# Optimization experiments

Measured on AMD Instinct MI355X. Metric: run time of the kernel, lower is better.

The kernel has to match this reference:

```python
import jax, jax.numpy as jnp
import numpy as np

B, L, K, H = 4, 256, 256, 768
KEY_SIZE, VAL_SIZE = 50000, 10000


def setup_inputs() -> dict:
    key = jax.random.key(0)
    k1, k2, k3, k4, k5, k6 = jax.random.split(key, 6)
    return {
        "hidden_state": jax.random.normal(k1, (B, L, H), dtype=jnp.float32),
        "key_seq": jax.random.randint(k2, (B, K), 0, KEY_SIZE),
        "value_matrix": jax.random.randint(k3, (B, L, K), 0, VAL_SIZE),
        "key_mask_matrix": jax.random.randint(k4, (B, L, K), 0, 2),
        "key_emb_table": jax.random.normal(k5, (KEY_SIZE, H), dtype=jnp.float32),
        "val_emb_table": jax.random.normal(k6, (VAL_SIZE, H), dtype=jnp.float32),
    }


def reference(hidden_state, key_seq, value_matrix, key_mask_matrix,
              key_emb_table, val_emb_table):
    temper = jnp.asarray(H, jnp.float32) ** 0.5
    # embedding lookups
    embedding_key = key_emb_table[key_seq]            # [B, K, H]
    embedding_val = val_emb_table[value_matrix]       # [B, L, K, H]
    # scores: hidden [B,L,H] x key [B,K,H] -> [B,L,K]
    u = jnp.einsum('blh,bkh->blk', hidden_state, embedding_key) / temper
    mask = jnp.clip(key_mask_matrix, 0, 1).astype(jnp.float32)
    delta_exp_u = jnp.exp(u) * mask                   # masked exp
    sum_delta = jnp.sum(delta_exp_u, axis=2, keepdims=True)
    p = delta_exp_u / (sum_delta + 1e-10)             # masked softmax [B,L,K]
    # weighted value sum (avoids the original's [H,B,L,K] broadcast+permute)
    o = jnp.einsum('blk,blkh->blh', p, embedding_val)
    return o + hidden_state
```

## Files before the change

kernel.cpp:

```cpp
#include <hip/hip_runtime.h>
#include <math.h>

typedef float    f32x2 __attribute__((ext_vector_type(2)));
typedef float    f32x4 __attribute__((ext_vector_type(4)));
typedef _Float16 f16x2 __attribute__((ext_vector_type(2)));

static constexpr int B_ = 4;
static constexpr int L_ = 256;
static constexpr int K_ = 256;
static constexpr int H_ = 768;
static constexpr int H2_ = H_ / 2;
static constexpr int VAL_SIZE_ = 10000;
static constexpr float INV_TEMPER = 0.03608439182435161f;

__device__ __forceinline__ unsigned pack_f16x2(float a, float b) {
  f16x2 p = {(_Float16)a, (_Float16)b};
  return __builtin_bit_cast(unsigned, p);
}
__device__ __forceinline__ float fdot2u(unsigned a, unsigned b, float c) {
#if __has_builtin(__builtin_amdgcn_fdot2)
  return __builtin_amdgcn_fdot2(__builtin_bit_cast(f16x2, a),
                                __builtin_bit_cast(f16x2, b), c, false);
#else
  f16x2 va = __builtin_bit_cast(f16x2, a);
  f16x2 vb = __builtin_bit_cast(f16x2, b);
  return c + (float)va.x * (float)vb.x + (float)va.y * (float)vb.y;
#endif
}

__device__ __forceinline__ float4 nt_load4(const float* p) {
  f32x4 v = __builtin_nontemporal_load(reinterpret_cast<const f32x4*>(p));
  return make_float4(v.x, v.y, v.z, v.w);
}

#if __has_builtin(__builtin_amdgcn_cvt_pk_fp8_f32)
#define HW_FP8_ENC 1
#endif
#if __has_builtin(__builtin_amdgcn_cvt_pk_f32_fp8)
#define HW_FP8_DEC 1
#endif

__device__ __forceinline__ unsigned fp8_enc1(float f) {
  unsigned s = (__float_as_uint(f) >> 31) << 7;
  float af = fminf(fabsf(f), 448.0f);
  unsigned em;
  if (af < 0.015625f) {
    em = (unsigned)rintf(af * 512.0f);
  } else {
    unsigned m = __float_as_uint(af);
    m += 0x7ffffu + ((m >> 20) & 1u);
    em = (m >> 20) - (120u << 3);
  }
  return s | em;
}
__device__ __forceinline__ float fp8_dec1(unsigned b) {
  unsigned em = b & 0x7fu;
  unsigned sbit = (b & 0x80u) << 24;
  float n = __uint_as_float(sbit | ((em + 960u) << 20));
  float sub = __uint_as_float(sbit | 0x3F800000u) * (float)em * 0.001953125f;
  return em >= 8u ? n : sub;
}
__device__ __forceinline__ unsigned fp8_enc4(float a, float b, float c, float d) {
#ifdef HW_FP8_ENC
  int w = 0;
  w = __builtin_amdgcn_cvt_pk_fp8_f32(a, b, w, false);
  w = __builtin_amdgcn_cvt_pk_fp8_f32(c, d, w, true);
  return (unsigned)w;
#else
  return fp8_enc1(a) | (fp8_enc1(b) << 8) | (fp8_enc1(c) << 16) | (fp8_enc1(d) << 24);
#endif
}
__device__ __forceinline__ void fp8_dec4(unsigned w, float* o) {
#ifdef HW_FP8_DEC
  f32x2 lo = __builtin_amdgcn_cvt_pk_f32_fp8((int)w, false);
  f32x2 hi = __builtin_amdgcn_cvt_pk_f32_fp8((int)w, true);
  o[0] = lo.x; o[1] = lo.y; o[2] = hi.x; o[3] = hi.y;
#else
  o[0] = fp8_dec1(w & 0xffu);
  o[1] = fp8_dec1((w >> 8) & 0xffu);
  o[2] = fp8_dec1((w >> 16) & 0xffu);
  o[3] = fp8_dec1(w >> 24);
#endif
}

static constexpr int TBLK = (K_ / 64) * (H_ / 64) * B_;
static constexpr int SBLK = (L_ / 4) * B_;
static constexpr int CBLK = (VAL_SIZE_ * H_) / 4096;

__global__ __launch_bounds__(256)
void k_prep(const int* __restrict__ key_seq,
            const float* __restrict__ key_emb,
            const float* __restrict__ vtab,
            unsigned* __restrict__ ET2,
            unsigned char* __restrict__ VT8) {
  __shared__ float tile[64][65];
  const int t = threadIdx.x;

  if (blockIdx.x >= TBLK) {
    const size_t base = (size_t)(blockIdx.x - TBLK) * 4096;
#pragma unroll
    for (int c = 0; c < 4; ++c) {
      const size_t e0 = base + (size_t)c * 1024 + (size_t)t * 4;
      const float4 a = nt_load4(vtab + e0);
      *reinterpret_cast<unsigned*>(VT8 + e0) = fp8_enc4(a.x, a.y, a.z, a.w);
    }
    return;
  }

  const int blk  = blockIdx.x;
  const int kb   = (blk % (K_ / 64)) * 64;
  const int hb   = ((blk / (K_ / 64)) % (H_ / 64)) * 64;
  const int b    = blk / ((K_ / 64) * (H_ / 64));
  const int sub  = t >> 6;
  const int lane = t & 63;

#pragma unroll
  for (int p = 0; p < 16; ++p) {
    const int kl  = p * 4 + sub;
    const int row = key_seq[b * K_ + kb + kl];
    tile[kl][lane] = key_emb[(size_t)row * H_ + hb + lane];
  }
  __syncthreads();
#pragma unroll
  for (int p = 0; p < 8; ++p) {
    const int hl2 = p * 4 + sub;
    ET2[((size_t)b * H2_ + (hb >> 1) + hl2) * K_ + kb + lane] =
        pack_f16x2(tile[lane][2 * hl2], tile[lane][2 * hl2 + 1]);
  }
}

__global__ __launch_bounds__(512)
void k_scores_pv(const float* __restrict__ hidden,
                 const unsigned* __restrict__ ET2,
                 const int* __restrict__ mask,
                 const int* __restrict__ vmat,
                 const unsigned char* __restrict__ VT8,
                 float* __restrict__ out) {
  __shared__ unsigned hid2[4 * H2_];
  __shared__ float4   part[4][256];
  __shared__ int      vmat_lds[4][K_];
  __shared__ float    pw[4][K_];
  __shared__ int      vidx[4][K_];
  __shared__ float    osum[4][H_];
  __shared__ int      nrow[4];

  const int t  = threadIdx.x;
  const int l0 = (blockIdx.x & 63) * 4;
  const int b  = blockIdx.x >> 6;

  const float* hsrc = hidden + ((size_t)b * L_ + l0) * H_;
  for (int i = t; i < 4 * H2_; i += 512) {
    const float2 hv = *reinterpret_cast<const float2*>(hsrc + 2 * i);
    hid2[i] = pack_f16x2(hv.x, hv.y);
  }
  if (t >= 256) {
    const int i  = t - 256;
    const int r  = i >> 6;
    const int c4 = (i & 63) * 4;
    *reinterpret_cast<int4*>(&vmat_lds[r][c4]) =
        *reinterpret_cast<const int4*>(vmat + ((size_t)b * L_ + l0 + r) * K_ + c4);
  }
  __syncthreads();

  if (t < 256) {
    const int kq = t & 63;
    const int hq = t >> 6;
    float4 acc[4];
#pragma unroll
    for (int l = 0; l < 4; ++l) acc[l] = make_float4(0.f, 0.f, 0.f, 0.f);

    const unsigned* etp =
        ET2 + (size_t)b * H2_ * K_ + (size_t)(hq * 96) * K_ + kq * 4;
    const int hbase2 = hq * 96;
#pragma unroll 4
    for (int hh = 0; hh < 96; ++hh) {
      const uint4 e = *reinterpret_cast<const uint4*>(etp + (size_t)hh * K_);
#pragma unroll
      for (int l = 0; l < 4; ++l) {
        const unsigned hv2 = hid2[l * H2_ + hbase2 + hh];
        acc[l].x = fdot2u(e.x, hv2, acc[l].x);
        acc[l].y = fdot2u(e.y, hv2, acc[l].y);
        acc[l].z = fdot2u(e.z, hv2, acc[l].z);
        acc[l].w = fdot2u(e.w, hv2, acc[l].w);
      }
    }
#pragma unroll
    for (int l = 0; l < 4; ++l) part[l][t] = acc[l];
  }
  __syncthreads();

  if (t < 256) {
    const int kq2 = t & 63;
    const int l2  = t >> 6;
    float4 a = part[l2][kq2];
    const float4 b1 = part[l2][64 + kq2];
    const float4 c  = part[l2][128 + kq2];
    const float4 d  = part[l2][192 + kq2];
    a.x += b1.x + c.x + d.x;
    a.y += b1.y + c.y + d.y;
    a.z += b1.z + c.z + d.z;
    a.w += b1.w + c.w + d.w;

    const int lrow = l0 + l2;
    const int4 m4 = *reinterpret_cast<const int4*>(
        mask + ((size_t)b * L_ + lrow) * K_ + kq2 * 4);
    float ex[4];
    ex[0] = (m4.x > 0) ? expf(a.x * INV_TEMPER) : 0.f;
    ex[1] = (m4.y > 0) ? expf(a.y * INV_TEMPER) : 0.f;
    ex[2] = (m4.z > 0) ? expf(a.z * INV_TEMPER) : 0.f;
    ex[3] = (m4.w > 0) ? expf(a.w * INV_TEMPER) : 0.f;

    float s = ex[0] + ex[1] + ex[2] + ex[3];
#pragma unroll
    for (int off = 32; off > 0; off >>= 1) s += __shfl_down(s, off);
    const float tot = __shfl(s, 0) + 1e-10f;
    const float rtot = 1.0f / tot;

    const unsigned long long lt = (1ull << kq2) - 1ull;
    unsigned long long m[4];
    int run = 0;
    int pos[4];
#pragma unroll
    for (int cc = 0; cc < 4; ++cc) {
      m[cc] = __ballot(ex[cc] != 0.f);
      pos[cc] = run + (int)__popcll(m[cc] & lt);
      run += (int)__popcll(m[cc]);
    }
#pragma unroll
    for (int cc = 0; cc < 4; ++cc) {
      if (ex[cc] != 0.f) {
        pw[l2][pos[cc]]   = ex[cc] * rtot;
        vidx[l2][pos[cc]] = vmat_lds[l2][kq2 * 4 + cc];
      }
    }
    if (kq2 == 0) nrow[l2] = run;
  }
  __syncthreads();

  const int w    = t >> 6;
  const int lane = t & 63;
  const int r    = w & 3;
  const int half = w >> 2;
  const int n    = nrow[r];

  float acc[12];
#pragma unroll
  for (int i = 0; i < 12; ++i) acc[i] = 0.f;

#pragma unroll 4
  for (int j = half; j < n; j += 2) {
    const float wgt = pw[r][j];
    const int   idx = vidx[r][j];
    const uint3 v = *reinterpret_cast<const uint3*>(
        VT8 + (size_t)idx * H_ + lane * 12);
    float f[12];
    fp8_dec4(v.x, f);
    fp8_dec4(v.y, f + 4);
    fp8_dec4(v.z, f + 8);
#pragma unroll
    for (int i = 0; i < 12; ++i) acc[i] += wgt * f[i];
  }

  if (half == 0) {
#pragma unroll
    for (int c = 0; c < 3; ++c)
      *reinterpret_cast<float4*>(&osum[r][lane * 12 + c * 4]) =
          make_float4(acc[c * 4], acc[c * 4 + 1], acc[c * 4 + 2], acc[c * 4 + 3]);
  }
  __syncthreads();
  if (half == 1) {
#pragma unroll
    for (int i = 0; i < 12; ++i) osum[r][lane * 12 + i] += acc[i];
  }
  __syncthreads();

  if (half == 1) {
    const float* hrow = hidden + ((size_t)b * L_ + l0 + r) * H_;
    float*       orow = out    + ((size_t)b * L_ + l0 + r) * H_;
#pragma unroll
    for (int c = 0; c < 3; ++c) {
      const int h0 = c * 256 + lane * 4;
      const float4 ov = *reinterpret_cast<const float4*>(&osum[r][h0]);
      const float4 hv = *reinterpret_cast<const float4*>(hrow + h0);
      *reinterpret_cast<float4*>(orow + h0) =
          make_float4(ov.x + hv.x, ov.y + hv.y, ov.z + hv.z, ov.w + hv.w);
    }
  }
}

extern "C" void kernel_launch(void* const* d_in, const int* in_sizes, int n_in,
                              void* d_out, int out_size, void* d_ws, size_t ws_size,
                              hipStream_t stream) {
  (void)in_sizes; (void)n_in; (void)out_size; (void)ws_size;
  const float* hidden  = (const float*)d_in[0];
  const int*   key_seq = (const int*)d_in[1];
  const int*   vmat    = (const int*)d_in[2];
  const int*   mask    = (const int*)d_in[3];
  const float* key_emb = (const float*)d_in[4];
  const float* val_emb = (const float*)d_in[5];
  float* out = (float*)d_out;

  unsigned char* VT8 = (unsigned char*)d_ws;
  unsigned*      ET2 = (unsigned*)(VT8 + (size_t)VAL_SIZE_ * H_);

  k_prep<<<TBLK + CBLK, 256, 0, stream>>>(key_seq, key_emb, val_emb, ET2, VT8);
  k_scores_pv<<<SBLK, 512, 0, stream>>>(hidden, ET2, mask, vmat, VT8, out);
}
```

Before: 39.46 us.

## Process two query rows per block with 8-way H split and 4-way PV split

Halves the rows handled by each block of the fused scores/PV kernel (2 instead of 4), doubling the grid to 512 blocks. All 512 threads now compute scores by splitting H into 8 slices, and four waves per row share the value-gather loop, with the partial sums reduced through shared memory. The aim is more blocks for occupancy across CUs and less idle time for half the threads in the score phase. In exchange, each key-embedding tile is reused across only 2 rows, so ET2 traffic per output row doubles.

```diff
diff --git a/kernel.cpp b/kernel.cpp
--- a/kernel.cpp
+++ b/kernel.cpp
@@ -84,7 +84,7 @@
 }
 
 static constexpr int TBLK = (K_ / 64) * (H_ / 64) * B_;
-static constexpr int SBLK = (L_ / 4) * B_;
+static constexpr int SBLK = (L_ / 2) * B_;
 static constexpr int CBLK = (VAL_SIZE_ * H_) / 4096;
 
 __global__ __launch_bounds__(256)
@@ -136,24 +136,24 @@
                  const int* __restrict__ vmat,
                  const unsigned char* __restrict__ VT8,
                  float* __restrict__ out) {
-  __shared__ unsigned hid2[4 * H2_];
-  __shared__ float4   part[4][256];
-  __shared__ int      vmat_lds[4][K_];
-  __shared__ float    pw[4][K_];
-  __shared__ int      vidx[4][K_];
-  __shared__ float    osum[4][H_];
-  __shared__ int      nrow[4];
+  __shared__ unsigned hid2[2 * H2_];
+  __shared__ float4   part[2][512];
+  __shared__ int      vmat_lds[2][K_];
+  __shared__ float    pw[2][K_];
+  __shared__ int      vidx[2][K_];
+  __shared__ float    osum[2][2][H_];
+  __shared__ int      nrow[2];
 
   const int t  = threadIdx.x;
-  const int l0 = (blockIdx.x & 63) * 4;
-  const int b  = blockIdx.x >> 6;
+  const int l0 = (blockIdx.x & 127) * 2;
+  const int b  = blockIdx.x >> 7;
 
   const float* hsrc = hidden + ((size_t)b * L_ + l0) * H_;
-  for (int i = t; i < 4 * H2_; i += 512) {
+  for (int i = t; i < 2 * H2_; i += 512) {
     const float2 hv = *reinterpret_cast<const float2*>(hsrc + 2 * i);
     hid2[i] = pack_f16x2(hv.x, hv.y);
   }
-  if (t >= 256) {
+  if (t >= 256 && t < 384) {
     const int i  = t - 256;
     const int r  = i >> 6;
     const int c4 = (i & 63) * 4;
@@ -162,21 +162,21 @@
   }
   __syncthreads();
 
-  if (t < 256) {
+  {
     const int kq = t & 63;
     const int hq = t >> 6;
-    float4 acc[4];
-#pragma unroll
-    for (int l = 0; l < 4; ++l) acc[l] = make_float4(0.f, 0.f, 0.f, 0.f);
+    float4 acc[2];
+#pragma unroll
+    for (int l = 0; l < 2; ++l) acc[l] = make_float4(0.f, 0.f, 0.f, 0.f);
 
     const unsigned* etp =
-        ET2 + (size_t)b * H2_ * K_ + (size_t)(hq * 96) * K_ + kq * 4;
-    const int hbase2 = hq * 96;
+        ET2 + (size_t)b * H2_ * K_ + (size_t)(hq * 48) * K_ + kq * 4;
+    const int hbase2 = hq * 48;
 #pragma unroll 4
-    for (int hh = 0; hh < 96; ++hh) {
+    for (int hh = 0; hh < 48; ++hh) {
       const uint4 e = *reinterpret_cast<const uint4*>(etp + (size_t)hh * K_);
 #pragma unroll
-      for (int l = 0; l < 4; ++l) {
+      for (int l = 0; l < 2; ++l) {
         const unsigned hv2 = hid2[l * H2_ + hbase2 + hh];
         acc[l].x = fdot2u(e.x, hv2, acc[l].x);
         acc[l].y = fdot2u(e.y, hv2, acc[l].y);
@@ -185,21 +185,19 @@
       }
     }
 #pragma unroll
-    for (int l = 0; l < 4; ++l) part[l][t] = acc[l];
-  }
-  __syncthreads();
-
-  if (t < 256) {
+    for (int l = 0; l < 2; ++l) part[l][t] = acc[l];
+  }
+  __syncthreads();
+
+  if (t < 128) {
     const int kq2 = t & 63;
     const int l2  = t >> 6;
     float4 a = part[l2][kq2];
-    const float4 b1 = part[l2][64 + kq2];
-    const float4 c  = part[l2][128 + kq2];
-    const float4 d  = part[l2][192 + kq2];
-    a.x += b1.x + c.x + d.x;
-    a.y += b1.y + c.y + d.y;
-    a.z += b1.z + c.z + d.z;
-    a.w += b1.w + c.w + d.w;
+#pragma unroll
+    for (int c = 1; c < 8; ++c) {
+      const float4 pc = part[l2][c * 64 + kq2];
+      a.x += pc.x; a.y += pc.y; a.z += pc.z; a.w += pc.w;
+    }
 
     const int lrow = l0 + l2;
     const int4 m4 = *reinterpret_cast<const int4*>(
@@ -239,8 +237,8 @@
 
   const int w    = t >> 6;
   const int lane = t & 63;
-  const int r    = w & 3;
-  const int half = w >> 2;
+  const int r    = w & 1;
+  const int q    = w >> 1;
   const int n    = nrow[r];
 
   float acc[12];
@@ -248,7 +246,7 @@
   for (int i = 0; i < 12; ++i) acc[i] = 0.f;
 
 #pragma unroll 4
-  for (int j = half; j < n; j += 2) {
+  for (int j = q; j < n; j += 4) {
     const float wgt = pw[r][j];
     const int   idx = vidx[r][j];
     const uint3 v = *reinterpret_cast<const uint3*>(
@@ -261,29 +259,31 @@
     for (int i = 0; i < 12; ++i) acc[i] += wgt * f[i];
   }
 
-  if (half == 0) {
+  if (q < 2) {
 #pragma unroll
     for (int c = 0; c < 3; ++c)
-      *reinterpret_cast<float4*>(&osum[r][lane * 12 + c * 4]) =
+      *reinterpret_cast<float4*>(&osum[r][q][lane * 12 + c * 4]) =
           make_float4(acc[c * 4], acc[c * 4 + 1], acc[c * 4 + 2], acc[c * 4 + 3]);
   }
   __syncthreads();
-  if (half == 1) {
-#pragma unroll
-    for (int i = 0; i < 12; ++i) osum[r][lane * 12 + i] += acc[i];
-  }
-  __syncthreads();
-
-  if (half == 1) {
+  if (q >= 2) {
+#pragma unroll
+    for (int i = 0; i < 12; ++i) osum[r][q - 2][lane * 12 + i] += acc[i];
+  }
+  __syncthreads();
+
+  if (q == 0) {
     const float* hrow = hidden + ((size_t)b * L_ + l0 + r) * H_;
     float*       orow = out    + ((size_t)b * L_ + l0 + r) * H_;
 #pragma unroll
     for (int c = 0; c < 3; ++c) {
       const int h0 = c * 256 + lane * 4;
-      const float4 ov = *reinterpret_cast<const float4*>(&osum[r][h0]);
+      const float4 o0 = *reinterpret_cast<const float4*>(&osum[r][0][h0]);
+      const float4 o1 = *reinterpret_cast<const float4*>(&osum[r][1][h0]);
       const float4 hv = *reinterpret_cast<const float4*>(hrow + h0);
       *reinterpret_cast<float4*>(orow + h0) =
-          make_float4(ov.x + hv.x, ov.y + hv.y, ov.z + hv.z, ov.w + hv.w);
+          make_float4(o0.x + o1.x + hv.x, o0.y + o1.y + hv.y,
+                      o0.z + o1.z + hv.z, o0.w + o1.w + hv.w);
     }
   }
 }
```

New measurement: 35.06 us. 11.2% less time.
